# Kernel tuning notes

Measured on AMD Instinct MI355X. Metric: run time of the kernel, lower is better.

The kernel has to match this reference:

```python
import jax, jax.numpy as jnp
import numpy as np
import math

EPS = 1e-5
NEG_SLOPE = 0.2

def _patches(x, k=3, s=2):
    # x: (N, C, H, W) -> (N, C, k*k, Ho, Wo); VALID padding, stride s
    N, C = x.shape[0], x.shape[1]
    p = jax.lax.conv_general_dilated_patches(x, (k, k), (s, s), 'VALID')
    return p.reshape(N, C, k * k, p.shape[2], p.shape[3])

def _pacconv(x, guide, w, b, k=3):
    # PacConv2d (gaussian kernel, smooth_kernel_type='none', no normalization)
    xp = _patches(x)                              # (N,Cin,K2,Ho,Wo)
    gp = _patches(guide)                          # (N,Cg,K2,Ho,Wo)
    ctr = (k * k) // 2
    d = gp - gp[:, :, ctr:ctr + 1]
    ker = jnp.exp(-0.5 * jnp.sum(d * d, axis=1, keepdims=True))  # (N,1,K2,Ho,Wo)
    out = jnp.einsum('nckhw,ock->nohw', xp * ker,
                     w.reshape(w.shape[0], w.shape[1], k * k))
    return out + b[None, :, None, None]

def _conv(x, w, b):
    out = jax.lax.conv_general_dilated(x, w, (2, 2), 'VALID',
                                       dimension_numbers=('NCHW', 'OIHW', 'NCHW'))
    return out + b[None, :, None, None]

def _avgpool(x):
    s = jax.lax.reduce_window(x, 0.0, jax.lax.add, (1, 1, 3, 3), (1, 1, 2, 2), 'VALID')
    return s / 9.0

def _lrelu(x):
    return jnp.where(x >= 0, x, NEG_SLOPE * x)

def _bn(x, g, b):
    # training-mode BatchNorm2d (batch stats, biased variance)
    m = jnp.mean(x, axis=(0, 2, 3), keepdims=True)
    v = jnp.mean((x - m) ** 2, axis=(0, 2, 3), keepdims=True)
    xn = (x - m) * jax.lax.rsqrt(v + EPS)
    return xn * g[None, :, None, None] + b[None, :, None, None]

def setup_inputs() -> dict:
    key = jax.random.key(0)
    ks = jax.random.split(key, 12)
    N, Cin, H = 128, 1, 120
    x = jax.random.normal(ks[0], (N, Cin, H, H), jnp.float32)
    guide = jax.random.uniform(ks[1], (N, 1, H, H), jnp.float32)
    def wconv(k, co, ci):
        return jax.random.normal(k, (co, ci, 3, 3), jnp.float32) * (1.0 / math.sqrt(ci * 9))
    w1, b1 = wconv(ks[2], 32, Cin), jnp.zeros((32,), jnp.float32)
    w2, b2 = wconv(ks[3], 64, 32), jnp.zeros((64,), jnp.float32)
    w3, b3 = wconv(ks[4], 128, 64), jnp.zeros((128,), jnp.float32)
    w4, b4 = wconv(ks[5], 256, 128), jnp.zeros((256,), jnp.float32)
    g2, be2 = jnp.ones((64,), jnp.float32), jnp.zeros((64,), jnp.float32)
    g3, be3 = jnp.ones((128,), jnp.float32), jnp.zeros((128,), jnp.float32)
    g4, be4 = jnp.ones((256,), jnp.float32), jnp.zeros((256,), jnp.float32)
    wadv = jax.random.normal(ks[6], (1, 9216), jnp.float32)  # EqualLinear raw weight
    badv = jnp.ones((1,), jnp.float32)                        # bias_init=1
    return {"x": x, "guide": guide, "w1": w1, "b1": b1, "w2": w2, "b2": b2,
            "w3": w3, "b3": b3, "w4": w4, "b4": b4, "g2": g2, "be2": be2,
            "g3": g3, "be3": be3, "g4": g4, "be4": be4, "wadv": wadv, "badv": badv}

def reference(x, guide, w1, b1, w2, b2, w3, b3, w4, b4,
              g2, be2, g3, be3, g4, be4, wadv, badv):
    out = _lrelu(_conv(x, w1, b1))                 # (N,32,59,59)
    guide = _avgpool(guide)                        # (N,1,59,59)
    out = _bn(_lrelu(_pacconv(out, guide, w2, b2)), g2, be2)   # (N,64,29,29)
    guide = _avgpool(guide)                        # (N,1,29,29)
    out = _bn(_lrelu(_pacconv(out, guide, w3, b3)), g3, be3)   # (N,128,14,14)
    guide = _avgpool(guide)                        # (N,1,14,14)
    out = _bn(_lrelu(_pacconv(out, guide, w4, b4)), g4, be4)   # (N,256,6,6)
    flat = out.reshape(out.shape[0], -1)           # (N,9216)
    scale = 1.0 / math.sqrt(9216)
    validity = flat @ (wadv * scale).T + badv      # EqualLinear, lr_mul=1
    return validity
```

## Files before the change

kernel.cpp:

```cpp
#include <hip/hip_runtime.h>
#include <hip/hip_bf16.h>

#define EPSBN 1e-5f
#define NEG_SLOPE 0.2f

using f32x4  = __attribute__((ext_vector_type(4))) float;
using bf16x8 = __attribute__((ext_vector_type(8))) short;

#define O_Y1B     0
#define O_G1      7129088
#define O_Y2B     7574656
#define O_G2      11019392
#define O_WKB2    11127040
#define O_WKB3    11136256
#define O_WKB4    11173120
#define O_WADVR   11320576
#define O_ACC     11329792
#define O_G3      11336960
#define O_Y3B     11362048
#define O_Y4B     12967680
#define A_ACC2    0
#define A_ACC3    1024
#define A_ACC4    3072

__device__ __forceinline__ unsigned short f2bf(float f) {
  union { __hip_bfloat16 b; unsigned short u; } cv;
  cv.b = __float2bfloat16(f);
  return cv.u;
}
__device__ __forceinline__ float bf2f(unsigned short u) {
  union { unsigned int i; float f; } x; x.i = (unsigned int)u << 16; return x.f;
}

#define CONV1_B 7552
#define AVG1_B  1741
#define RPK_B   1548
#define ZERO_B  7
__global__ __launch_bounds__(256) void prep_kernel(
    const float* __restrict__ x, const float* __restrict__ gd,
    const float* __restrict__ w1, const float* __restrict__ b1,
    const float* __restrict__ w2, const float* __restrict__ w3,
    const float* __restrict__ w4, const float* __restrict__ wadv,
    float* __restrict__ ws) {
  const int bi = blockIdx.x, tid = threadIdx.x;
  __shared__ float xs[360];
  __shared__ float wsm[320];
  __shared__ unsigned short ysm[1888];
  if (bi < CONV1_B) {
    const int n = bi / 59, oh = bi % 59;
    for (int i = tid; i < 320; i += 256)
      wsm[i] = (i < 288) ? w1[(i & 31) * 9 + (i >> 5)] : b1[i - 288];
    const float* src = x + ((size_t)n * 120 + oh * 2) * 120;
    for (int i = tid; i < 360; i += 256) xs[i] = src[i];
    __syncthreads();
    const int co = tid & 31;
    const int ow0 = (tid >> 5) * 8;
    float w[9];
#pragma unroll
    for (int k = 0; k < 9; ++k) w[k] = wsm[k * 32 + co];
    const float bias = wsm[288 + co];
#pragma unroll
    for (int j = 0; j < 8; ++j) {
      int ow = ow0 + j;
      if (ow < 59) {
        float acc = bias;
#pragma unroll
        for (int kh = 0; kh < 3; ++kh)
#pragma unroll
          for (int kw = 0; kw < 3; ++kw)
            acc += xs[kh * 120 + ow * 2 + kw] * w[kh * 3 + kw];
        acc = acc >= 0.0f ? acc : NEG_SLOPE * acc;
        ysm[ow * 32 + co] = f2bf(acc);
      }
    }
    __syncthreads();
    unsigned int* dst = (unsigned int*)((unsigned short*)(ws + O_Y1B) +
                                        (size_t)(n * 59 + oh) * 1888);
    const unsigned int* s2 = (const unsigned int*)ysm;
    for (int i = tid; i < 944; i += 256) dst[i] = s2[i];
  } else if (bi < CONV1_B + AVG1_B) {
    int idx = (bi - CONV1_B) * 256 + tid;
    if (idx < 445568) {
      int ow = idx % 59; int t = idx / 59; int oh = t % 59; int n = t / 59;
      const float* gb = gd + (n * 120 + oh * 2) * 120 + ow * 2;
      float s = 0.0f;
#pragma unroll
      for (int kh = 0; kh < 3; ++kh)
#pragma unroll
        for (int kw = 0; kw < 3; ++kw) s += gb[kh * 120 + kw];
      ws[O_G1 + idx] = s * (1.0f / 9.0f);
    }
  } else if (bi < CONV1_B + AVG1_B + RPK_B) {
    int idx = (bi - CONV1_B - AVG1_B) * 256 + tid;
    if (idx < 18432) {
      int kk = idx & 31; int t = idx >> 5; int co = t & 63; int tap = t >> 6;
      ((unsigned short*)(ws + O_WKB2))[idx] = f2bf(w2[(co * 32 + kk) * 9 + tap]);
    } else if (idx < 92160) {
      int i = idx - 18432;
      int kk = i & 31; int t = i >> 5; int co = t & 127; int t3 = t >> 7;
      int kc = t3 & 1; int tap = t3 >> 1;
      ((unsigned short*)(ws + O_WKB3))[i] = f2bf(w3[(co * 64 + kc * 32 + kk) * 9 + tap]);
    } else if (idx < 387072) {
      int i = idx - 92160;
      int kk = i & 31; int t = i >> 5; int co = t & 255; int t3 = t >> 8;
      int kc = t3 & 3; int tap = t3 >> 2;
      ((unsigned short*)(ws + O_WKB4))[i] = f2bf(w4[(co * 128 + kc * 32 + kk) * 9 + tap]);
    } else if (idx < 396288) {
      int i = idx - 387072;
      int c = i & 255; int hw = i >> 8;
      ws[O_WADVR + i] = wadv[c * 36 + hw] * (1.0f / 96.0f);
    }
  } else {
    int idx = (bi - CONV1_B - AVG1_B - RPK_B) * 256 + tid;
    if (idx * 4 < 7168) {
      float4 z = {0.0f, 0.0f, 0.0f, 0.0f};
      *reinterpret_cast<float4*>(ws + O_ACC + idx * 4) = z;
    }
  }
}

template <int CI, int CO, int HI, int HO, int NWM, int NWN, bool BN_IN,
          int NBLK, int MINW, bool POOL>
__global__ __launch_bounds__(256, MINW)
void pac_kernel(const unsigned short* __restrict__ xb, const float* __restrict__ g,
                const float* __restrict__ wkb_f, const float* __restrict__ b,
                const float* __restrict__ gamma, const float* __restrict__ beta,
                const float* __restrict__ accin, float invM,
                unsigned short* __restrict__ yb, float* __restrict__ accout,
                const float* __restrict__ pin, float* __restrict__ pgout,
                int PHI, int PHO, int PTOT) {
  constexpr int KC   = CI / 32;
  constexpr int S    = 9 * KC;
  constexpr int MBLK = NWM * 32;
  constexpr int BSZ  = BN_IN ? CI : 1;
  const unsigned short* wkb = (const unsigned short*)wkb_f;

  const int tid = threadIdx.x;
  const int bi  = blockIdx.x;

  if constexpr (POOL) {
    if (bi >= NBLK) {
      int idx = (bi - NBLK) * 256 + tid;
      if (idx < PTOT) {
        int ow = idx % PHO; int t = idx / PHO; int oh = t % PHO; int n = t / PHO;
        const float* gb = pin + (n * PHI + oh * 2) * PHI + ow * 2;
        float s = 0.0f;
#pragma unroll
        for (int kh = 0; kh < 3; ++kh)
#pragma unroll
          for (int kw = 0; kw < 3; ++kw) s += gb[kh * PHI + kw];
        pgout[idx] = s * (1.0f / 9.0f);
      }
      return;
    }
  }

  __shared__ float bscl[BSZ], bshl[BSZ];
  __shared__ float ps[NWM][CO * 2];
  __shared__ unsigned short ytile[4][2048];

  const int lane = tid & 63;
  const int wv   = tid >> 6;
  const int wm   = wv / NWN, wn = wv % NWN;
  const int blk  = bi;
  const int l15  = lane & 15;
  const int g8   = (lane >> 4) * 8;

  if constexpr (BN_IN) {
    if (tid < CI) {
      float s = 0.0f, q = 0.0f;
#pragma unroll
      for (int sl = 0; sl < 8; ++sl) {
        s += accin[(sl * CI + tid) * 2 + 0];
        q += accin[(sl * CI + tid) * 2 + 1];
      }
      float m = s * invM;
      float var = q * invM - m * m;
      float sc = gamma[tid] * rsqrtf(var + EPSBN);
      bscl[tid] = sc;
      bshl[tid] = beta[tid] - m * sc;
    }
    __syncthreads();
  }

  float kk[2][9];
  int   xo[2];
#pragma unroll
  for (int mt = 0; mt < 2; ++mt) {
    int p  = blk * MBLK + wm * 32 + mt * 16 + l15;
    int ow = p % HO, oh = (p / HO) % HO, n = p / (HO * HO);
    const float* gn = g + n * (HI * HI);
    float gc = gn[(oh * 2 + 1) * HI + ow * 2 + 1];
#pragma unroll
    for (int t = 0; t < 9; ++t) {
      float d = gn[(oh * 2 + t / 3) * HI + ow * 2 + (t % 3)] - gc;
      kk[mt][t] = __expf(-0.5f * d * d);
    }
    xo[mt] = ((n * HI + oh * 2) * HI + ow * 2) * CI;
  }

  f32x4 acc[2][4];
#pragma unroll
  for (int nt = 0; nt < 4; ++nt) {
    float bv = b[wn * 64 + nt * 16 + l15];
#pragma unroll
    for (int mt = 0; mt < 2; ++mt) acc[mt][nt] = (f32x4){bv, bv, bv, bv};
  }

#pragma unroll
  for (int i = 0; i < S; ++i) {
    const int t  = i / KC;
    const int kc = i % KC;
    const int xoff = ((t / 3) * HI + (t % 3)) * CI + kc * 32 + g8;
    bf16x8 bfv[4];
#pragma unroll
    for (int nt = 0; nt < 4; ++nt)
      bfv[nt] = *(const bf16x8*)(wkb + ((size_t)i * CO + wn * 64 + nt * 16 + l15) * 32 + g8);
    bf16x8 af[2];
#pragma unroll
    for (int mt = 0; mt < 2; ++mt) {
      bf16x8 u = *(const bf16x8*)(xb + xo[mt] + xoff);
      float v[8];
#pragma unroll
      for (int j = 0; j < 8; ++j) v[j] = bf2f((unsigned short)u[j]);
      if constexpr (BN_IN) {
        const int c0 = kc * 32 + g8;
#pragma unroll
        for (int j = 0; j < 8; ++j) v[j] = v[j] * bscl[c0 + j] + bshl[c0 + j];
      }
      const float kv = kk[mt][t];
#pragma unroll
      for (int j = 0; j < 8; ++j) v[j] *= kv;
#pragma unroll
      for (int j = 0; j < 8; ++j) af[mt][j] = (short)f2bf(v[j]);
    }
#pragma unroll
    for (int mt = 0; mt < 2; ++mt)
#pragma unroll
      for (int nt = 0; nt < 4; ++nt)
        acc[mt][nt] = __builtin_amdgcn_mfma_f32_16x16x32_bf16(af[mt], bfv[nt], acc[mt][nt], 0, 0, 0);
  }

#pragma unroll
  for (int nt = 0; nt < 4; ++nt) {
    const int co = wn * 64 + nt * 16 + l15;
    float s = 0.0f, q = 0.0f;
#pragma unroll
    for (int mt = 0; mt < 2; ++mt)
#pragma unroll
      for (int r = 0; r < 4; ++r) {
        float v = acc[mt][nt][r];
        v = v >= 0.0f ? v : NEG_SLOPE * v;
        int row = mt * 16 + ((lane >> 4) << 2) + r;
        ytile[wv][row * 64 + nt * 16 + l15] = f2bf(v);
        s += v; q += v * v;
      }
    s += __shfl_xor(s, 16, 64); q += __shfl_xor(q, 16, 64);
    s += __shfl_xor(s, 32, 64); q += __shfl_xor(q, 32, 64);
    if (l15 == lane) { ps[wm][co * 2 + 0] = s; ps[wm][co * 2 + 1] = q; }
  }
  __syncthreads();
  {
    unsigned short* dbase = yb + (size_t)(blk * MBLK + wm * 32) * CO + wn * 64;
    const uint4* srcT = (const uint4*)ytile[wv];
#pragma unroll
    for (int i = 0; i < 4; ++i) {
      int row = i * 8 + (lane >> 3);
      int u4  = lane & 7;
      *(uint4*)(dbase + (size_t)row * CO + u4 * 8) = srcT[row * 8 + u4];
    }
  }
  if (tid < CO) {
    float s = 0.0f, q = 0.0f;
#pragma unroll
    for (int wmx = 0; wmx < NWM; ++wmx) { s += ps[wmx][tid * 2]; q += ps[wmx][tid * 2 + 1]; }
    atomicAdd(&accout[((blk & 7) * CO + tid) * 2 + 0], s);
    atomicAdd(&accout[((blk & 7) * CO + tid) * 2 + 1], q);
  }
}

__global__ void linear_kernel(const unsigned short* __restrict__ y4b,
                              const float* __restrict__ acc4,
                              const float* __restrict__ bg4, const float* __restrict__ bb4,
                              const float* __restrict__ wadvr, const float* __restrict__ badv,
                              float* __restrict__ out) {
  int n = blockIdx.x, t = threadIdx.x;
  float s0 = 0.0f, q0 = 0.0f;
#pragma unroll
  for (int sl = 0; sl < 8; ++sl) {
    s0 += acc4[(sl * 256 + t) * 2 + 0];
    q0 += acc4[(sl * 256 + t) * 2 + 1];
  }
  float m = s0 * (1.0f / 4608.0f);
  float var = q0 * (1.0f / 4608.0f) - m * m;
  float sc = bg4[t] * rsqrtf(var + EPSBN);
  float sh = bb4[t] - m * sc;
  float s = 0.0f;
  for (int j = t; j < 9216; j += 256)
    s += (bf2f(y4b[n * 9216 + j]) * sc + sh) * wadvr[j];
  __shared__ float ss[256];
  ss[t] = s; __syncthreads();
  for (int off = 128; off > 0; off >>= 1) {
    if (t < off) ss[t] += ss[t + off];
    __syncthreads();
  }
  if (t == 0) out[n] = ss[0] + badv[0];
}

extern "C" void kernel_launch(void* const* d_in, const int* in_sizes, int n_in,
                              void* d_out, int out_size, void* d_ws, size_t ws_size,
                              hipStream_t stream) {
  const float* x    = (const float*)d_in[0];
  const float* gd   = (const float*)d_in[1];
  const float* w1   = (const float*)d_in[2];
  const float* b1   = (const float*)d_in[3];
  const float* w2   = (const float*)d_in[4];
  const float* b2   = (const float*)d_in[5];
  const float* w3   = (const float*)d_in[6];
  const float* b3   = (const float*)d_in[7];
  const float* w4   = (const float*)d_in[8];
  const float* b4   = (const float*)d_in[9];
  const float* bg2  = (const float*)d_in[10];
  const float* bb2  = (const float*)d_in[11];
  const float* bg3  = (const float*)d_in[12];
  const float* bb3  = (const float*)d_in[13];
  const float* bg4  = (const float*)d_in[14];
  const float* bb4  = (const float*)d_in[15];
  const float* wadv = (const float*)d_in[16];
  const float* badv = (const float*)d_in[17];
  float* out = (float*)d_out;
  float* ws  = (float*)d_ws;

  unsigned short* y1b = (unsigned short*)(ws + O_Y1B);
  unsigned short* y2b = (unsigned short*)(ws + O_Y2B);
  unsigned short* y3b = (unsigned short*)(ws + O_Y3B);
  unsigned short* y4b = (unsigned short*)(ws + O_Y4B);
  float* acc2 = ws + O_ACC + A_ACC2;
  float* acc3 = ws + O_ACC + A_ACC3;
  float* acc4 = ws + O_ACC + A_ACC4;

  prep_kernel<<<CONV1_B + AVG1_B + RPK_B + ZERO_B, 256, 0, stream>>>(
      x, gd, w1, b1, w2, w3, w4, wadv, ws);

  pac_kernel<32, 64, 59, 29, 4, 1, false, 841, 3, true>
      <<<1262, 256, 0, stream>>>(y1b, ws + O_G1, ws + O_WKB2, b2,
                                 nullptr, nullptr, nullptr, 0.0f,
                                 y2b, acc2,
                                 ws + O_G1, ws + O_G2, 59, 29, 107648);

  pac_kernel<64, 128, 29, 14, 2, 2, true, 392, 2, true>
      <<<490, 256, 0, stream>>>(y2b, ws + O_G2, ws + O_WKB3, b3,
                                bg2, bb2, acc2, 1.0f / 107648.0f,
                                y3b, acc3,
                                ws + O_G2, ws + O_G3, 29, 14, 25088);

  pac_kernel<128, 256, 14, 6, 1, 4, true, 144, 2, false>
      <<<144, 256, 0, stream>>>(y3b, ws + O_G3, ws + O_WKB4, b4,
                                bg3, bb3, acc3, 1.0f / 25088.0f,
                                y4b, acc4,
                                nullptr, nullptr, 0, 0, 0);

  linear_kernel<<<128, 256, 0, stream>>>(y4b, acc4, bg4, bb4,
                                         ws + O_WADVR, badv, out);
}
```

Before: 105.4 us.

## Fuse all stages into one persistent cooperative kernel with grid syncs

Replaces the five separate kernel launches with a single cooperative persistent kernel of at most 512 blocks. Each block loops over virtual block indices for every stage, and grid.sync() separates the stages. The aim is to remove launch overhead and inter-kernel gaps. In exchange, the grid is capped below the original block counts, occupancy is limited by launch_bounds(256,2) and shared memory is shared across stages. The original multi-kernel path is kept as a fallback if the cooperative launch fails.

```diff
diff --git a/kernel.cpp b/kernel.cpp
--- a/kernel.cpp
+++ b/kernel.cpp
@@ -1,5 +1,8 @@
 #include <hip/hip_runtime.h>
+#include <hip/hip_cooperative_groups.h>
 #include <hip/hip_bf16.h>
+
+namespace cg = cooperative_groups;
 
 #define EPSBN 1e-5f
 #define NEG_SLOPE 0.2f
@@ -32,25 +35,24 @@
   union { unsigned int i; float f; } x; x.i = (unsigned int)u << 16; return x.f;
 }
 
-#define CONV1_B 7552
-#define AVG1_B  1741
-#define RPK_B   1548
-#define ZERO_B  7
-__global__ __launch_bounds__(256) void prep_kernel(
-    const float* __restrict__ x, const float* __restrict__ gd,
-    const float* __restrict__ w1, const float* __restrict__ b1,
-    const float* __restrict__ w2, const float* __restrict__ w3,
-    const float* __restrict__ w4, const float* __restrict__ wadv,
-    float* __restrict__ ws) {
-  const int bi = blockIdx.x, tid = threadIdx.x;
-  __shared__ float xs[360];
-  __shared__ float wsm[320];
-  __shared__ unsigned short ysm[1888];
-  if (bi < CONV1_B) {
-    const int n = bi / 59, oh = bi % 59;
+struct KParams {
+  const float *x, *gd, *w1, *b1, *w2, *b2, *w3, *b3, *w4, *b4;
+  const float *bg2, *bb2, *bg3, *bb3, *bg4, *bb4, *wadv, *badv;
+  float* out;
+  float* ws;
+};
+
+
+__device__ __forceinline__ void prep_body(int vb, int tid, const KParams& p, char* smem) {
+  float* ws = p.ws;
+  if (vb < 7552) {
+    float* xs  = (float*)smem;
+    float* wsm = (float*)(smem + 1536);
+    unsigned short* ysm = (unsigned short*)(smem + 2944);
+    const int n = vb / 59, oh = vb % 59;
     for (int i = tid; i < 320; i += 256)
-      wsm[i] = (i < 288) ? w1[(i & 31) * 9 + (i >> 5)] : b1[i - 288];
-    const float* src = x + ((size_t)n * 120 + oh * 2) * 120;
+      wsm[i] = (i < 288) ? p.w1[(i & 31) * 9 + (i >> 5)] : p.b1[i - 288];
+    const float* src = p.x + ((size_t)n * 120 + oh * 2) * 120;
     for (int i = tid; i < 360; i += 256) xs[i] = src[i];
     __syncthreads();
     const int co = tid & 31;
@@ -78,11 +80,12 @@
                                         (size_t)(n * 59 + oh) * 1888);
     const unsigned int* s2 = (const unsigned int*)ysm;
     for (int i = tid; i < 944; i += 256) dst[i] = s2[i];
-  } else if (bi < CONV1_B + AVG1_B) {
-    int idx = (bi - CONV1_B) * 256 + tid;
+    __syncthreads();
+  } else if (vb < 9293) {
+    int idx = (vb - 7552) * 256 + tid;
     if (idx < 445568) {
       int ow = idx % 59; int t = idx / 59; int oh = t % 59; int n = t / 59;
-      const float* gb = gd + (n * 120 + oh * 2) * 120 + ow * 2;
+      const float* gb = p.gd + (n * 120 + oh * 2) * 120 + ow * 2;
       float s = 0.0f;
 #pragma unroll
       for (int kh = 0; kh < 3; ++kh)
@@ -90,28 +93,28 @@
         for (int kw = 0; kw < 3; ++kw) s += gb[kh * 120 + kw];
       ws[O_G1 + idx] = s * (1.0f / 9.0f);
     }
-  } else if (bi < CONV1_B + AVG1_B + RPK_B) {
-    int idx = (bi - CONV1_B - AVG1_B) * 256 + tid;
+  } else if (vb < 10841) {
+    int idx = (vb - 9293) * 256 + tid;
     if (idx < 18432) {
       int kk = idx & 31; int t = idx >> 5; int co = t & 63; int tap = t >> 6;
-      ((unsigned short*)(ws + O_WKB2))[idx] = f2bf(w2[(co * 32 + kk) * 9 + tap]);
+      ((unsigned short*)(ws + O_WKB2))[idx] = f2bf(p.w2[(co * 32 + kk) * 9 + tap]);
     } else if (idx < 92160) {
       int i = idx - 18432;
       int kk = i & 31; int t = i >> 5; int co = t & 127; int t3 = t >> 7;
       int kc = t3 & 1; int tap = t3 >> 1;
-      ((unsigned short*)(ws + O_WKB3))[i] = f2bf(w3[(co * 64 + kc * 32 + kk) * 9 + tap]);
+      ((unsigned short*)(ws + O_WKB3))[i] = f2bf(p.w3[(co * 64 + kc * 32 + kk) * 9 + tap]);
     } else if (idx < 387072) {
       int i = idx - 92160;
       int kk = i & 31; int t = i >> 5; int co = t & 255; int t3 = t >> 8;
       int kc = t3 & 3; int tap = t3 >> 2;
-      ((unsigned short*)(ws + O_WKB4))[i] = f2bf(w4[(co * 128 + kc * 32 + kk) * 9 + tap]);
+      ((unsigned short*)(ws + O_WKB4))[i] = f2bf(p.w4[(co * 128 + kc * 32 + kk) * 9 + tap]);
     } else if (idx < 396288) {
       int i = idx - 387072;
       int c = i & 255; int hw = i >> 8;
-      ws[O_WADVR + i] = wadv[c * 36 + hw] * (1.0f / 96.0f);
+      ws[O_WADVR + i] = p.wadv[c * 36 + hw] * (1.0f / 96.0f);
     }
   } else {
-    int idx = (bi - CONV1_B - AVG1_B - RPK_B) * 256 + tid;
+    int idx = (vb - 10841) * 256 + tid;
     if (idx * 4 < 7168) {
       float4 z = {0.0f, 0.0f, 0.0f, 0.0f};
       *reinterpret_cast<float4*>(ws + O_ACC + idx * 4) = z;
@@ -119,50 +122,42 @@
   }
 }
 
-template <int CI, int CO, int HI, int HO, int NWM, int NWN, bool BN_IN,
-          int NBLK, int MINW, bool POOL>
-__global__ __launch_bounds__(256, MINW)
-void pac_kernel(const unsigned short* __restrict__ xb, const float* __restrict__ g,
-                const float* __restrict__ wkb_f, const float* __restrict__ b,
-                const float* __restrict__ gamma, const float* __restrict__ beta,
-                const float* __restrict__ accin, float invM,
-                unsigned short* __restrict__ yb, float* __restrict__ accout,
-                const float* __restrict__ pin, float* __restrict__ pgout,
-                int PHI, int PHO, int PTOT) {
+__device__ __forceinline__ void pool_body(const float* __restrict__ pin,
+                                          float* __restrict__ pgout,
+                                          int PHI, int PHO, int vb, int tid, int PTOT) {
+  int idx = vb * 256 + tid;
+  if (idx < PTOT) {
+    int ow = idx % PHO; int t = idx / PHO; int oh = t % PHO; int n = t / PHO;
+    const float* gb = pin + (n * PHI + oh * 2) * PHI + ow * 2;
+    float s = 0.0f;
+#pragma unroll
+    for (int kh = 0; kh < 3; ++kh)
+#pragma unroll
+      for (int kw = 0; kw < 3; ++kw) s += gb[kh * PHI + kw];
+    pgout[idx] = s * (1.0f / 9.0f);
+  }
+}
+
+template <int CI, int CO, int HI, int HO, int NWM, int NWN, bool BN_IN>
+__device__ __forceinline__ void pac_body(
+    char* smem, int blk, int tid,
+    const unsigned short* __restrict__ xb, const float* __restrict__ g,
+    const unsigned short* __restrict__ wkb, const float* __restrict__ b,
+    const float* __restrict__ gamma, const float* __restrict__ beta,
+    const float* __restrict__ accin, float invM,
+    unsigned short* __restrict__ yb, float* __restrict__ accout) {
   constexpr int KC   = CI / 32;
   constexpr int S    = 9 * KC;
   constexpr int MBLK = NWM * 32;
-  constexpr int BSZ  = BN_IN ? CI : 1;
-  const unsigned short* wkb = (const unsigned short*)wkb_f;
-
-  const int tid = threadIdx.x;
-  const int bi  = blockIdx.x;
-
-  if constexpr (POOL) {
-    if (bi >= NBLK) {
-      int idx = (bi - NBLK) * 256 + tid;
-      if (idx < PTOT) {
-        int ow = idx % PHO; int t = idx / PHO; int oh = t % PHO; int n = t / PHO;
-        const float* gb = pin + (n * PHI + oh * 2) * PHI + ow * 2;
-        float s = 0.0f;
-#pragma unroll
-        for (int kh = 0; kh < 3; ++kh)
-#pragma unroll
-          for (int kw = 0; kw < 3; ++kw) s += gb[kh * PHI + kw];
-        pgout[idx] = s * (1.0f / 9.0f);
-      }
-      return;
-    }
-  }
-
-  __shared__ float bscl[BSZ], bshl[BSZ];
-  __shared__ float ps[NWM][CO * 2];
-  __shared__ unsigned short ytile[4][2048];
+
+  unsigned short* ytile = (unsigned short*)smem;
+  float* ps   = (float*)(smem + 16384);
+  float* bscl = (float*)(smem + 18432);
+  float* bshl = bscl + CI;
 
   const int lane = tid & 63;
   const int wv   = tid >> 6;
   const int wm   = wv / NWN, wn = wv % NWN;
-  const int blk  = bi;
   const int l15  = lane & 15;
   const int g8   = (lane >> 4) * 8;
 
@@ -187,8 +182,8 @@
   int   xo[2];
 #pragma unroll
   for (int mt = 0; mt < 2; ++mt) {
-    int p  = blk * MBLK + wm * 32 + mt * 16 + l15;
-    int ow = p % HO, oh = (p / HO) % HO, n = p / (HO * HO);
+    int pp = blk * MBLK + wm * 32 + mt * 16 + l15;
+    int ow = pp % HO, oh = (pp / HO) % HO, n = pp / (HO * HO);
     const float* gn = g + n * (HI * HI);
     float gc = gn[(oh * 2 + 1) * HI + ow * 2 + 1];
 #pragma unroll
@@ -252,17 +247,17 @@
         float v = acc[mt][nt][r];
         v = v >= 0.0f ? v : NEG_SLOPE * v;
         int row = mt * 16 + ((lane >> 4) << 2) + r;
-        ytile[wv][row * 64 + nt * 16 + l15] = f2bf(v);
+        ytile[wv * 2048 + row * 64 + nt * 16 + l15] = f2bf(v);
         s += v; q += v * v;
       }
     s += __shfl_xor(s, 16, 64); q += __shfl_xor(q, 16, 64);
     s += __shfl_xor(s, 32, 64); q += __shfl_xor(q, 32, 64);
-    if (l15 == lane) { ps[wm][co * 2 + 0] = s; ps[wm][co * 2 + 1] = q; }
+    if (l15 == lane) { ps[wm * (CO * 2) + co * 2 + 0] = s; ps[wm * (CO * 2) + co * 2 + 1] = q; }
   }
   __syncthreads();
   {
     unsigned short* dbase = yb + (size_t)(blk * MBLK + wm * 32) * CO + wn * 64;
-    const uint4* srcT = (const uint4*)ytile[wv];
+    const uint4* srcT = (const uint4*)(ytile + wv * 2048);
 #pragma unroll
     for (int i = 0; i < 4; ++i) {
       int row = i * 8 + (lane >> 3);
@@ -273,18 +268,20 @@
   if (tid < CO) {
     float s = 0.0f, q = 0.0f;
 #pragma unroll
-    for (int wmx = 0; wmx < NWM; ++wmx) { s += ps[wmx][tid * 2]; q += ps[wmx][tid * 2 + 1]; }
+    for (int wmx = 0; wmx < NWM; ++wmx) {
+      s += ps[wmx * (CO * 2) + tid * 2];
+      q += ps[wmx * (CO * 2) + tid * 2 + 1];
+    }
     atomicAdd(&accout[((blk & 7) * CO + tid) * 2 + 0], s);
     atomicAdd(&accout[((blk & 7) * CO + tid) * 2 + 1], q);
   }
-}
-
-__global__ void linear_kernel(const unsigned short* __restrict__ y4b,
-                              const float* __restrict__ acc4,
-                              const float* __restrict__ bg4, const float* __restrict__ bb4,
-                              const float* __restrict__ wadvr, const float* __restrict__ badv,
-                              float* __restrict__ out) {
-  int n = blockIdx.x, t = threadIdx.x;
+  __syncthreads();
+}
+
+__device__ __forceinline__ void linear_body(char* smem, int n, int t, const KParams& p) {
+  float* ws = p.ws;
+  const unsigned short* y4b = (const unsigned short*)(ws + O_Y4B);
+  const float* acc4 = ws + O_ACC + A_ACC4;
   float s0 = 0.0f, q0 = 0.0f;
 #pragma unroll
   for (int sl = 0; sl < 8; ++sl) {
@@ -293,73 +290,160 @@
   }
   float m = s0 * (1.0f / 4608.0f);
   float var = q0 * (1.0f / 4608.0f) - m * m;
-  float sc = bg4[t] * rsqrtf(var + EPSBN);
-  float sh = bb4[t] - m * sc;
+  float sc = p.bg4[t] * rsqrtf(var + EPSBN);
+  float sh = p.bb4[t] - m * sc;
+  const float* wadvr = ws + O_WADVR;
   float s = 0.0f;
   for (int j = t; j < 9216; j += 256)
     s += (bf2f(y4b[n * 9216 + j]) * sc + sh) * wadvr[j];
-  __shared__ float ss[256];
+  float* ss = (float*)smem;
   ss[t] = s; __syncthreads();
   for (int off = 128; off > 0; off >>= 1) {
     if (t < off) ss[t] += ss[t + off];
     __syncthreads();
   }
-  if (t == 0) out[n] = ss[0] + badv[0];
-}
-
-extern "C" void kernel_launch(void* const* d_in, const int* in_sizes, int n_in,
-                              void* d_out, int out_size, void* d_ws, size_t ws_size,
-                              hipStream_t stream) {
-  const float* x    = (const float*)d_in[0];
-  const float* gd   = (const float*)d_in[1];
-  const float* w1   = (const float*)d_in[2];
-  const float* b1   = (const float*)d_in[3];
-  const float* w2   = (const float*)d_in[4];
-  const float* b2   = (const float*)d_in[5];
-  const float* w3   = (const float*)d_in[6];
-  const float* b3   = (const float*)d_in[7];
-  const float* w4   = (const float*)d_in[8];
-  const float* b4   = (const float*)d_in[9];
-  const float* bg2  = (const float*)d_in[10];
-  const float* bb2  = (const float*)d_in[11];
-  const float* bg3  = (const float*)d_in[12];
-  const float* bb3  = (const float*)d_in[13];
-  const float* bg4  = (const float*)d_in[14];
-  const float* bb4  = (const float*)d_in[15];
-  const float* wadv = (const float*)d_in[16];
-  const float* badv = (const float*)d_in[17];
-  float* out = (float*)d_out;
-  float* ws  = (float*)d_ws;
+  if (t == 0) p.out[n] = ss[0] + p.badv[0];
+  __syncthreads();
+}
+
+__global__ __launch_bounds__(256, 2) void net_kernel(KParams p) {
+  __shared__ __align__(16) char smem[19456];
+  cg::grid_group grid = cg::this_grid();
+  const int tid = threadIdx.x;
+  const int bid = blockIdx.x;
+  const int gsz = gridDim.x;
+  float* ws = p.ws;
 
   unsigned short* y1b = (unsigned short*)(ws + O_Y1B);
   unsigned short* y2b = (unsigned short*)(ws + O_Y2B);
   unsigned short* y3b = (unsigned short*)(ws + O_Y3B);
   unsigned short* y4b = (unsigned short*)(ws + O_Y4B);
+  const unsigned short* wkb2 = (const unsigned short*)(ws + O_WKB2);
+  const unsigned short* wkb3 = (const unsigned short*)(ws + O_WKB3);
+  const unsigned short* wkb4 = (const unsigned short*)(ws + O_WKB4);
   float* acc2 = ws + O_ACC + A_ACC2;
   float* acc3 = ws + O_ACC + A_ACC3;
   float* acc4 = ws + O_ACC + A_ACC4;
 
-  prep_kernel<<<CONV1_B + AVG1_B + RPK_B + ZERO_B, 256, 0, stream>>>(
-      x, gd, w1, b1, w2, w3, w4, wadv, ws);
-
-  pac_kernel<32, 64, 59, 29, 4, 1, false, 841, 3, true>
-      <<<1262, 256, 0, stream>>>(y1b, ws + O_G1, ws + O_WKB2, b2,
-                                 nullptr, nullptr, nullptr, 0.0f,
-                                 y2b, acc2,
-                                 ws + O_G1, ws + O_G2, 59, 29, 107648);
-
-  pac_kernel<64, 128, 29, 14, 2, 2, true, 392, 2, true>
-      <<<490, 256, 0, stream>>>(y2b, ws + O_G2, ws + O_WKB3, b3,
-                                bg2, bb2, acc2, 1.0f / 107648.0f,
-                                y3b, acc3,
-                                ws + O_G2, ws + O_G3, 29, 14, 25088);
-
-  pac_kernel<128, 256, 14, 6, 1, 4, true, 144, 2, false>
-      <<<144, 256, 0, stream>>>(y3b, ws + O_G3, ws + O_WKB4, b4,
-                                bg3, bb3, acc3, 1.0f / 25088.0f,
-                                y4b, acc4,
-                                nullptr, nullptr, 0, 0, 0);
-
-  linear_kernel<<<128, 256, 0, stream>>>(y4b, acc4, bg4, bb4,
-                                         ws + O_WADVR, badv, out);
-}
+  for (int vb = bid; vb < 10848; vb += gsz) prep_body(vb, tid, p, smem);
+  grid.sync();
+
+  for (int vb = bid; vb < 1262; vb += gsz) {
+    if (vb < 841)
+      pac_body<32, 64, 59, 29, 4, 1, false>(smem, vb, tid, y1b, ws + O_G1, wkb2,
+                                            p.b2, nullptr, nullptr, nullptr, 0.0f,
+                                            y2b, acc2);
+    else
+      pool_body(ws + O_G1, ws + O_G2, 59, 29, vb - 841, tid, 107648);
+  }
+  grid.sync();
+
+  for (int vb = bid; vb < 490; vb += gsz) {
+    if (vb < 392)
+      pac_body<64, 128, 29, 14, 2, 2, true>(smem, vb, tid, y2b, ws + O_G2, wkb3,
+                                            p.b3, p.bg2, p.bb2, acc2, 1.0f / 107648.0f,
+                                            y3b, acc3);
+    else
+      pool_body(ws + O_G2, ws + O_G3, 29, 14, vb - 392, tid, 25088);
+  }
+  grid.sync();
+
+  for (int vb = bid; vb < 144; vb += gsz)
+    pac_body<128, 256, 14, 6, 1, 4, true>(smem, vb, tid, y3b, ws + O_G3, wkb4,
+                                          p.b4, p.bg3, p.bb3, acc3, 1.0f / 25088.0f,
+                                          y4b, acc4);
+  grid.sync();
+
+  for (int vb = bid; vb < 128; vb += gsz) linear_body(smem, vb, tid, p);
+}
+
+__global__ __launch_bounds__(256, 2) void k_prep(KParams p) {
+  __shared__ __align__(16) char smem[8192];
+  prep_body(blockIdx.x, threadIdx.x, p, smem);
+}
+__global__ __launch_bounds__(256, 2) void k_s1(KParams p) {
+  __shared__ __align__(16) char smem[19456];
+  float* ws = p.ws;
+  int vb = blockIdx.x;
+  if (vb < 841)
+    pac_body<32, 64, 59, 29, 4, 1, false>(smem, vb, threadIdx.x,
+        (unsigned short*)(ws + O_Y1B), ws + O_G1, (const unsigned short*)(ws + O_WKB2),
+        p.b2, nullptr, nullptr, nullptr, 0.0f,
+        (unsigned short*)(ws + O_Y2B), ws + O_ACC + A_ACC2);
+  else
+    pool_body(ws + O_G1, ws + O_G2, 59, 29, vb - 841, threadIdx.x, 107648);
+}
+__global__ __launch_bounds__(256, 2) void k_s2(KParams p) {
+  __shared__ __align__(16) char smem[19456];
+  float* ws = p.ws;
+  int vb = blockIdx.x;
+  if (vb < 392)
+    pac_body<64, 128, 29, 14, 2, 2, true>(smem, vb, threadIdx.x,
+        (unsigned short*)(ws + O_Y2B), ws + O_G2, (const unsigned short*)(ws + O_WKB3),
+        p.b3, p.bg2, p.bb2, ws + O_ACC + A_ACC2, 1.0f / 107648.0f,
+        (unsigned short*)(ws + O_Y3B), ws + O_ACC + A_ACC3);
+  else
+    pool_body(ws + O_G2, ws + O_G3, 29, 14, vb - 392, threadIdx.x, 25088);
+}
+__global__ __launch_bounds__(256, 2) void k_s3(KParams p) {
+  __shared__ __align__(16) char smem[19456];
+  float* ws = p.ws;
+  pac_body<128, 256, 14, 6, 1, 4, true>(smem, blockIdx.x, threadIdx.x,
+      (unsigned short*)(ws + O_Y3B), ws + O_G3, (const unsigned short*)(ws + O_WKB4),
+      p.b4, p.bg3, p.bb3, ws + O_ACC + A_ACC3, 1.0f / 25088.0f,
+      (unsigned short*)(ws + O_Y4B), ws + O_ACC + A_ACC4);
+}
+__global__ __launch_bounds__(256, 2) void k_s4(KParams p) {
+  __shared__ __align__(16) char smem[1024];
+  linear_body(smem, blockIdx.x, threadIdx.x, p);
+}
+
+extern "C" void kernel_launch(void* const* d_in, const int* in_sizes, int n_in,
+                              void* d_out, int out_size, void* d_ws, size_t ws_size,
+                              hipStream_t stream) {
+  KParams prm;
+  prm.x    = (const float*)d_in[0];
+  prm.gd   = (const float*)d_in[1];
+  prm.w1   = (const float*)d_in[2];
+  prm.b1   = (const float*)d_in[3];
+  prm.w2   = (const float*)d_in[4];
+  prm.b2   = (const float*)d_in[5];
+  prm.w3   = (const float*)d_in[6];
+  prm.b3   = (const float*)d_in[7];
+  prm.w4   = (const float*)d_in[8];
+  prm.b4   = (const float*)d_in[9];
+  prm.bg2  = (const float*)d_in[10];
+  prm.bb2  = (const float*)d_in[11];
+  prm.bg3  = (const float*)d_in[12];
+  prm.bb3  = (const float*)d_in[13];
+  prm.bg4  = (const float*)d_in[14];
+  prm.bb4  = (const float*)d_in[15];
+  prm.wadv = (const float*)d_in[16];
+  prm.badv = (const float*)d_in[17];
+  prm.out  = (float*)d_out;
+  prm.ws   = (float*)d_ws;
+
+  bool launched = false;
+  int dev = 0, numCU = 0, maxB = 0;
+  if (hipGetDevice(&dev) == hipSuccess &&
+      hipDeviceGetAttribute(&numCU, hipDeviceAttributeMultiprocessorCount, dev) == hipSuccess &&
+      hipOccupancyMaxActiveBlocksPerMultiprocessor(&maxB, (const void*)net_kernel, 256, 0) == hipSuccess &&
+      numCU > 0 && maxB > 0) {
+    long cap = (long)numCU * (long)maxB;
+    int grid = cap > 512 ? 512 : (int)cap;
+    if (grid >= 64) {
+      void* args[] = { (void*)&prm };
+      if (hipLaunchCooperativeKernel((const void*)net_kernel, dim3(grid), dim3(256),
+                                     args, 0, stream) == hipSuccess)
+        launched = true;
+    }
+  }
+
+  if (!launched) {
+    k_prep<<<10848, 256, 0, stream>>>(prm);
+    k_s1<<<1262, 256, 0, stream>>>(prm);
+    k_s2<<<490, 256, 0, stream>>>(prm);
+    k_s3<<<144, 256, 0, stream>>>(prm);
+    k_s4<<<128, 256, 0, stream>>>(prm);
+  }
+}
```

Result: slower. 364.9 us (+246.2%).
